# Performance work log

Measured on AMD Instinct MI355X. Metric: run time of the kernel, lower is better.

Reference implementation:

```python
import jax, jax.numpy as jnp
import numpy as np

# Soft decision tree: heap-ordered full binary tree.
# Inner node n (0-based heap index) has gate p_n = sigmoid(beta_n * (x @ W_n + b_n)).
# Children of n are 2n+1 (left, prob 1-p) and 2n+2 (right, prob p).

LMBDA = 0.1


def setup_inputs() -> dict:
    key = jax.random.key(0)
    k = jax.random.split(key, 6)
    B, IN, OUT, D = 8192, 2048, 100, 8
    N = 2 ** D - 1          # inner nodes = 255
    L = 2 ** D              # leaves = 256
    x = jax.random.normal(k[0], (B, IN), dtype=jnp.float32)
    labels = jax.random.randint(k[1], (B,), 0, OUT, dtype=jnp.int32)
    W = jax.random.normal(k[2], (N, IN), dtype=jnp.float32) * 0.02
    b = jax.random.normal(k[3], (N,), dtype=jnp.float32) * 0.02
    beta = jax.random.normal(k[4], (N,), dtype=jnp.float32)
    leaf_params = jax.random.normal(k[5], (L, OUT), dtype=jnp.float32)
    return {"x": x, "labels": labels, "W": W, "b": b, "beta": beta,
            "leaf_params": leaf_params}


def _tree_paths(p, depth):
    """p: [B, N] gate probs in heap order. Returns (inner_path [B,N], leaf_path [B,L])."""
    B = p.shape[0]
    path = jnp.ones((B, 1), p.dtype)
    inner_paths = []
    start = 0
    for d in range(depth):
        width = 2 ** d
        p_lvl = p[:, start:start + width]          # [B, width]
        inner_paths.append(path)                   # path prob arriving at each inner node
        left = path * (1.0 - p_lvl)
        right = path * p_lvl
        # interleave -> heap order of next level: [l0, r0, l1, r1, ...]
        path = jnp.stack([left, right], axis=-1).reshape(B, 2 * width)
        start += width
    return jnp.concatenate(inner_paths, axis=1), path


def reference(x, labels, W, b, beta, leaf_params):
    N = W.shape[0]
    D = int(np.log2(N + 1))            # max_depth
    OUT = leaf_params.shape[1]

    # All inner-node gates in one GEMM: sigmoid(beta * (x @ W^T + b))
    p = jax.nn.sigmoid(beta[None, :] * (x @ W.T + b[None, :]))   # [B, N]
    inner_path, leaf_path = _tree_paths(p, D)                    # [B,N], [B,L]

    # Leaf distributions: softmax over each leaf's params
    logQ = jax.nn.log_softmax(leaf_params, axis=-1)              # [L, OUT]
    Q = jnp.exp(logQ)                                            # [L, OUT]

    # y one-hot; TQ[b, l] = y_b . log Q_l
    y = jax.nn.one_hot(labels, OUT, dtype=x.dtype)               # [B, OUT]
    TQ = y @ logQ.T                                              # [B, L]
    loss = jnp.mean(jnp.sum(leaf_path * TQ, axis=1))
    neg_loss = -loss

    # Penalty: only inner nodes whose children are also inner (depth 1..D-1)
    n_pen = 2 ** (D - 1) - 1
    alpha = jnp.sum(p * inner_path, axis=0) / jnp.sum(inner_path, axis=0)  # [N]
    node_idx = np.arange(N)
    depths = np.floor(np.log2(node_idx + 1)).astype(np.int32) + 1
    lmbda_arr = jnp.asarray(LMBDA * (2.0 ** (-depths)), dtype=x.dtype)     # [N]
    a = alpha[:n_pen]
    C = -jnp.sum(lmbda_arr[:n_pen] * 0.5 * (jnp.log(a) + jnp.log1p(-a)))

    # Output: leaf distribution of the max-path-prob leaf per sample
    best_leaf = jnp.argmax(leaf_path, axis=1)                    # [B]
    output = Q[best_leaf]                                        # [B, OUT]

    return neg_loss, output, C
```

## Files before the change

kernel.cpp:

```cpp
#include <hip/hip_runtime.h>
#include <math.h>

typedef __attribute__((ext_vector_type(4)))  short short4v;
typedef __attribute__((ext_vector_type(8)))  short short8v;
typedef __attribute__((ext_vector_type(4)))  float f32x4;

#define OFF_LOGQT 256
#define OFF_Q     25856
#define OFF_WHI   51456
#define OFF_WLO   313600
#define OFF_P0    575744
#define PART_STRIDE 2097152

__device__ __forceinline__ unsigned short f2bf(float f) {
    unsigned int b = __float_as_uint(f);
    unsigned int r = (b + 0x7FFFu + ((b >> 16) & 1u)) >> 16;
    return (unsigned short)r;
}
__device__ __forceinline__ float bf2f(unsigned short u) {
    return __uint_as_float(((unsigned int)u) << 16);
}

__global__ __launch_bounds__(256) void k_prep(const float* __restrict__ W,
                                              unsigned short* __restrict__ whi,
                                              unsigned short* __restrict__ wlo,
                                              const float* __restrict__ lp,
                                              float* __restrict__ logQT,
                                              float* __restrict__ Q,
                                              float* __restrict__ accum)
{
    const int bx = blockIdx.x, tid = threadIdx.x;
    if (bx < 256) {
        if (bx == 0) accum[tid] = 0.f;
        int g = (bx * 256 + tid) * 8;
        int row = g >> 11;
        unsigned short h[8], l[8];
        if (row < 255) {
            const float* src = W + (size_t)row * 2048 + (g & 2047);
            float4 v0 = *(const float4*)src;
            float4 v1 = *(const float4*)(src + 4);
            float vv[8] = {v0.x, v0.y, v0.z, v0.w, v1.x, v1.y, v1.z, v1.w};
#pragma unroll
            for (int j = 0; j < 8; ++j) {
                h[j] = f2bf(vv[j]);
                l[j] = f2bf(vv[j] - bf2f(h[j]));
            }
        } else {
#pragma unroll
            for (int j = 0; j < 8; ++j) { h[j] = 0; l[j] = 0; }
        }
#pragma unroll
        for (int j = 0; j < 8; ++j) { whi[g + j] = h[j]; wlo[g + j] = l[j]; }
    } else {
        int w = tid >> 6, lane = tid & 63;
        int r = (bx - 256) * 4 + w;
        float v0 = (lane < 100)      ? lp[r * 100 + lane]      : -INFINITY;
        float v1 = (lane + 64 < 100) ? lp[r * 100 + lane + 64] : -INFINITY;
        float m = fmaxf(v0, v1);
        for (int s = 32; s; s >>= 1) m = fmaxf(m, __shfl_xor(m, s));
        float e = 0.f;
        if (lane < 100)      e += expf(v0 - m);
        if (lane + 64 < 100) e += expf(v1 - m);
        for (int s = 32; s; s >>= 1) e += __shfl_xor(e, s);
        float logZ = m + logf(e);
        if (lane < 100) {
            float lq = v0 - logZ;
            Q[r * 100 + lane] = expf(lq);
            logQT[lane * 256 + r] = lq;
        }
        if (lane + 64 < 100) {
            float lq = v1 - logZ;
            Q[r * 100 + lane + 64] = expf(lq);
            logQT[(lane + 64) * 256 + r] = lq;
        }
    }
}

#define GBK 64
#define LDR 136

__global__ __launch_bounds__(256, 1) void k_gemm(const float* __restrict__ x,
                                                 const unsigned short* __restrict__ whi,
                                                 const unsigned short* __restrict__ wlo,
                                                 float* __restrict__ part,
                                                 int ksteps)
{
    __shared__ unsigned short As[128 * LDR];
    __shared__ unsigned short Bs[128 * LDR];

    const int tid  = threadIdx.x;
    const int w    = tid >> 6, lane = tid & 63;
    const int wm   = w >> 1, wn = w & 1;
    const int r16  = lane & 15, hi8 = (lane >> 4) * 8;
    const int row0 = blockIdx.x * 128;
    const int col0 = blockIdx.y * 128;
    const int kz   = blockIdx.z;
    const size_t kbase = (size_t)kz * ksteps * GBK;
    float* pdst = part + (size_t)kz * PART_STRIDE;

    f32x4 acc[4][4] = {};

    float4  aR[8];
    short8v bH[4], bL[4];

    auto GL = [&](int s) {
        const size_t k0 = kbase + (size_t)s * GBK;
#pragma unroll
        for (int i = 0; i < 8; ++i) {
            int g = tid + i * 256;
            int ar = g >> 4, ac = (g & 15) * 4;
            aR[i] = *(const float4*)(x + (size_t)(row0 + ar) * 2048 + k0 + ac);
        }
#pragma unroll
        for (int i = 0; i < 4; ++i) {
            int g = tid + i * 256;
            int br = g >> 3, bc = (g & 7) * 8;
            size_t wo = (size_t)(col0 + br) * 2048 + k0 + bc;
            bH[i] = *(const short8v*)(whi + wo);
            bL[i] = *(const short8v*)(wlo + wo);
        }
    };

    auto DSW = [&]() {
#pragma unroll
        for (int i = 0; i < 8; ++i) {
            int g = tid + i * 256;
            int ar = g >> 4, ac = (g & 15) * 4;
            float vv[4] = {aR[i].x, aR[i].y, aR[i].z, aR[i].w};
            short4v hv, lv;
#pragma unroll
            for (int j = 0; j < 4; ++j) {
                unsigned short hb = f2bf(vv[j]);
                hv[j] = (short)hb;
                lv[j] = (short)f2bf(vv[j] - bf2f(hb));
            }
            *(short4v*)&As[ar * LDR + ac]      = hv;
            *(short4v*)&As[ar * LDR + 64 + ac] = lv;
        }
#pragma unroll
        for (int i = 0; i < 4; ++i) {
            int g = tid + i * 256;
            int br = g >> 3, bc = (g & 7) * 8;
            *(short8v*)&Bs[br * LDR + bc]      = bH[i];
            *(short8v*)&Bs[br * LDR + 64 + bc] = bL[i];
        }
    };

    GL(0);
    for (int s = 0; s < ksteps; ++s) {
        DSW();
        __syncthreads();
        if (s + 1 < ksteps) GL(s + 1);
#pragma unroll
        for (int kk = 0; kk < 2; ++kk) {
            const int kc = kk * 32 + hi8;
            short8v ah[4], al[4];
#pragma unroll
            for (int fm = 0; fm < 4; ++fm) {
                int base = (wm * 64 + fm * 16 + r16) * LDR + kc;
                ah[fm] = *(const short8v*)&As[base];
                al[fm] = *(const short8v*)&As[base + 64];
            }
#pragma unroll
            for (int fn = 0; fn < 4; ++fn) {
                int bb = (wn * 64 + fn * 16 + r16) * LDR + kc;
                short8v bhh = *(const short8v*)&Bs[bb];
                short8v bll = *(const short8v*)&Bs[bb + 64];
#pragma unroll
                for (int fm = 0; fm < 4; ++fm) {
                    acc[fm][fn] = __builtin_amdgcn_mfma_f32_16x16x32_bf16(ah[fm], bhh, acc[fm][fn], 0, 0, 0);
                    acc[fm][fn] = __builtin_amdgcn_mfma_f32_16x16x32_bf16(ah[fm], bll, acc[fm][fn], 0, 0, 0);
                    acc[fm][fn] = __builtin_amdgcn_mfma_f32_16x16x32_bf16(al[fm], bhh, acc[fm][fn], 0, 0, 0);
                }
            }
        }
        __syncthreads();
    }

#pragma unroll
    for (int fm = 0; fm < 4; ++fm) {
#pragma unroll
        for (int fn = 0; fn < 4; ++fn) {
            int col = col0 + wn * 64 + fn * 16 + r16;
#pragma unroll
            for (int j = 0; j < 4; ++j) {
                int row = row0 + wm * 64 + fm * 16 + (lane >> 4) * 4 + j;
                pdst[(size_t)row * 256 + col] = acc[fm][fn][j];
            }
        }
    }
}

__global__ __launch_bounds__(256) void k_tree(const float* __restrict__ part, int npart,
                                              const float* __restrict__ bias,
                                              const float* __restrict__ beta,
                                              const int* __restrict__ labels,
                                              const float* __restrict__ logQT,
                                              const float* __restrict__ Q,
                                              float* __restrict__ accum,
                                              float* __restrict__ out)
{
    __shared__ float psh[4][256];
    __shared__ float redPI[4][128];
    __shared__ float redI[4][128];
    __shared__ float lossw[4];
    const int tid = threadIdx.x;
    const int w = tid >> 6, lane = tid & 63;
    const int c0 = lane * 4;

    float4 bi, be;
    if (lane < 63) {
        bi = *(const float4*)&bias[c0];
        be = *(const float4*)&beta[c0];
    } else {
        bi = make_float4(bias[252], bias[253], bias[254], 0.f);
        be = make_float4(beta[252], beta[253], beta[254], 0.f);
    }

    float aPI0 = 0.f, aPI1 = 0.f, aI0 = 0.f, aI1 = 0.f, lossAcc = 0.f;

    for (int rr = 0; rr < 2; ++rr) {
        int b = blockIdx.x * 8 + w * 2 + rr;

        float4 s = make_float4(0.f, 0.f, 0.f, 0.f);
        for (int z = 0; z < npart; ++z) {
            float4 v = *(const float4*)&part[(size_t)z * PART_STRIDE + (size_t)b * 256 + c0];
            s.x += v.x; s.y += v.y; s.z += v.z; s.w += v.w;
        }
        float4 pv;
        pv.x = 1.f / (1.f + expf(-be.x * (s.x + bi.x)));
        pv.y = 1.f / (1.f + expf(-be.y * (s.y + bi.y)));
        pv.z = 1.f / (1.f + expf(-be.z * (s.z + bi.z)));
        pv.w = 1.f / (1.f + expf(-be.w * (s.w + bi.w)));
        *(float4*)&psh[w][c0] = pv;
        asm volatile("s_waitcnt lgkmcnt(0)" ::: "memory");
        __builtin_amdgcn_sched_barrier(0);

        int label = labels[b];
        float4 tq = *(const float4*)&logQT[(size_t)label * 256 + c0];

        float prefix = 1.f;
#pragma unroll
        for (int d = 0; d < 6; ++d) {
            int node = (1 << d) - 1 + (lane >> (6 - d));
            float g = psh[w][node];
            prefix *= ((lane >> (5 - d)) & 1) ? g : (1.f - g);
        }
        float g6  = psh[w][63 + lane];
        float p60 = prefix * (1.f - g6), p61 = prefix * g6;
        float g7a = psh[w][127 + 2 * lane];
        float g7b = psh[w][128 + 2 * lane];
        float f0 = p60 * (1.f - g7a), f1 = p60 * g7a;
        float f2 = p61 * (1.f - g7b), f3 = p61 * g7b;

        float lsum = f0 * tq.x + f1 * tq.y + f2 * tq.z + f3 * tq.w;

        float best = f0; int bestIdx = c0;
        if (f1 > best) { best = f1; bestIdx = c0 + 1; }
        if (f2 > best) { best = f2; bestIdx = c0 + 2; }
        if (f3 > best) { best = f3; bestIdx = c0 + 3; }

        for (int sft = 32; sft; sft >>= 1) lsum += __shfl_xor(lsum, sft);
        for (int sft = 32; sft; sft >>= 1) {
            float ov = __shfl_xor(best, sft);
            int   oi = __shfl_xor(bestIdx, sft);
            if (ov > best || (ov == best && oi < bestIdx)) { best = ov; bestIdx = oi; }
        }
        lossAcc += lsum;

        {
            int n = lane;
            float f = 1.f;
            int cur = n;
            while (cur > 0) {
                int par = (cur - 1) >> 1;
                float g = psh[w][par];
                f *= (cur == 2 * par + 2) ? g : (1.f - g);
                cur = par;
            }
            aPI0 += psh[w][n] * f;
            aI0  += f;
        }
        if (lane < 63) {
            int n = lane + 64;
            float f = 1.f;
            int cur = n;
            while (cur > 0) {
                int par = (cur - 1) >> 1;
                float g = psh[w][par];
                f *= (cur == 2 * par + 2) ? g : (1.f - g);
                cur = par;
            }
            aPI1 += psh[w][n] * f;
            aI1  += f;
        }

        const float* qrow = Q + (size_t)bestIdx * 100;
        float* orow = out + 1 + (size_t)b * 100;
        orow[lane] = qrow[lane];
        if (lane < 36) orow[64 + lane] = qrow[64 + lane];
    }

    redPI[w][lane] = aPI0;           redI[w][lane] = aI0;
    redPI[w][64 + lane] = (lane < 63) ? aPI1 : 0.f;
    redI [w][64 + lane] = (lane < 63) ? aI1  : 0.f;
    if (lane == 0) lossw[w] = lossAcc;
    __syncthreads();
    if (tid < 127) {
        float sPI = redPI[0][tid] + redPI[1][tid] + redPI[2][tid] + redPI[3][tid];
        float sI  = redI [0][tid] + redI [1][tid] + redI [2][tid] + redI [3][tid];
        atomicAdd(&accum[1 + tid],   sPI);
        atomicAdd(&accum[128 + tid], sI);
    }
    if (tid == 128) {
        atomicAdd(&accum[0], lossw[0] + lossw[1] + lossw[2] + lossw[3]);
    }
}

__global__ __launch_bounds__(128) void k_final(const float* __restrict__ accum,
                                               float* __restrict__ out)
{
    __shared__ float s[128];
    int t = threadIdx.x;
    float term = 0.f;
    if (t < 127) {
        float a = accum[1 + t] / accum[128 + t];
        int depth = 32 - __clz(t + 1);
        float lmbda = 0.1f * exp2f(-(float)depth);
        term = -lmbda * 0.5f * (logf(a) + log1pf(-a));
    }
    s[t] = term;
    __syncthreads();
    if (t == 0) {
        float c = 0.f;
        for (int i = 0; i < 127; ++i) c += s[i];
        out[819201] = c;
        out[0] = -accum[0] / 8192.0f;
    }
}

extern "C" void kernel_launch(void* const* d_in, const int* in_sizes, int n_in,
                              void* d_out, int out_size, void* d_ws, size_t ws_size,
                              hipStream_t stream)
{
    const float* x      = (const float*)d_in[0];
    const int*   labels = (const int*)  d_in[1];
    const float* W      = (const float*)d_in[2];
    const float* bias   = (const float*)d_in[3];
    const float* beta   = (const float*)d_in[4];
    const float* leaf   = (const float*)d_in[5];
    float* out = (float*)d_out;
    float* ws  = (float*)d_ws;

    float*          accum = ws;
    float*          logQT = ws + OFF_LOGQT;
    float*          Q     = ws + OFF_Q;
    unsigned short* whi   = (unsigned short*)(ws + OFF_WHI);
    unsigned short* wlo   = (unsigned short*)(ws + OFF_WLO);
    float*          part  = ws + OFF_P0;

    auto need = [](int k) {
        return (size_t)(OFF_P0 + (size_t)k * PART_STRIDE) * sizeof(float);
    };
    int ksplit = (ws_size >= need(4)) ? 4 : (ws_size >= need(2)) ? 2 : 1;
    int ksteps = 32 / ksplit;

    k_prep<<<320, 256, 0, stream>>>(W, whi, wlo, leaf, logQT, Q, accum);
    k_gemm<<<dim3(64, 2, ksplit), 256, 0, stream>>>(x, whi, wlo, part, ksteps);
    k_tree<<<1024, 256, 0, stream>>>(part, ksplit, bias, beta, labels, logQT, Q, accum, out);
    k_final<<<1, 128, 0, stream>>>(accum, out);
}
```

Baseline: 194.0 us.

## Pre-split x into bf16 hi/lo and stream GEMM tiles via global_load_lds

Adds a prep pass that converts x into bf16 hi/lo arrays once, so the GEMM no longer does per-tile fp32-to-bf16 splitting in registers. A new GEMM kernel uses 64x256 tiles with direct global-to-LDS loads and two blocks per CU, keeping the old kernel as a fallback when the workspace is too small. The tree kernel now processes four rows per wave in half as many blocks. The cost is an extra full read and write of x (about 64MB of traffic), and the new GEMM has no software pipelining and unpadded LDS rows, so bank conflicts are possible.

```diff
diff --git a/kernel.cpp b/kernel.cpp
--- a/kernel.cpp
+++ b/kernel.cpp
@@ -9,7 +9,10 @@
 #define OFF_Q     25856
 #define OFF_WHI   51456
 #define OFF_WLO   313600
-#define OFF_P0    575744
+#define OFF_XHI   575744
+#define OFF_XLO   8964352
+#define OFF_PART_NEW 17352960
+#define OFF_PART_OLD 575744
 #define PART_STRIDE 2097152
 
 __device__ __forceinline__ unsigned short f2bf(float f) {
@@ -20,8 +23,17 @@
 __device__ __forceinline__ float bf2f(unsigned short u) {
     return __uint_as_float(((unsigned int)u) << 16);
 }
-
-__global__ __launch_bounds__(256) void k_prep(const float* __restrict__ W,
+__device__ __forceinline__ void gl16(const void* g, void* l) {
+    __builtin_amdgcn_global_load_lds(
+        (const __attribute__((address_space(1))) unsigned int*)g,
+        (__attribute__((address_space(3))) unsigned int*)l, 16, 0, 0);
+}
+
+__global__ __launch_bounds__(256) void k_prep(const float* __restrict__ x,
+                                              unsigned short* __restrict__ xhi,
+                                              unsigned short* __restrict__ xlo,
+                                              int nxblk,
+                                              const float* __restrict__ W,
                                               unsigned short* __restrict__ whi,
                                               unsigned short* __restrict__ wlo,
                                               const float* __restrict__ lp,
@@ -30,9 +42,27 @@
                                               float* __restrict__ accum)
 {
     const int bx = blockIdx.x, tid = threadIdx.x;
-    if (bx < 256) {
-        if (bx == 0) accum[tid] = 0.f;
-        int g = (bx * 256 + tid) * 8;
+    if (bx < nxblk) {
+        int g = bx * 2048 + tid * 8;
+        float4 v0 = *(const float4*)(x + g);
+        float4 v1 = *(const float4*)(x + g + 4);
+        float vv[8] = {v0.x, v0.y, v0.z, v0.w, v1.x, v1.y, v1.z, v1.w};
+        short4v h0, h1, l0, l1;
+#pragma unroll
+        for (int j = 0; j < 4; ++j) {
+            unsigned short hb = f2bf(vv[j]);
+            h0[j] = (short)hb; l0[j] = (short)f2bf(vv[j] - bf2f(hb));
+            unsigned short hb2 = f2bf(vv[j + 4]);
+            h1[j] = (short)hb2; l1[j] = (short)f2bf(vv[j + 4] - bf2f(hb2));
+        }
+        *(short4v*)(xhi + g) = h0;  *(short4v*)(xhi + g + 4) = h1;
+        *(short4v*)(xlo + g) = l0;  *(short4v*)(xlo + g + 4) = l1;
+        return;
+    }
+    const int bxx = bx - nxblk;
+    if (bxx < 256) {
+        if (bxx == 0) accum[tid] = 0.f;
+        int g = (bxx * 256 + tid) * 8;
         int row = g >> 11;
         unsigned short h[8], l[8];
         if (row < 255) {
@@ -53,7 +83,7 @@
         for (int j = 0; j < 8; ++j) { whi[g + j] = h[j]; wlo[g + j] = l[j]; }
     } else {
         int w = tid >> 6, lane = tid & 63;
-        int r = (bx - 256) * 4 + w;
+        int r = (bxx - 256) * 4 + w;
         float v0 = (lane < 100)      ? lp[r * 100 + lane]      : -INFINITY;
         float v1 = (lane + 64 < 100) ? lp[r * 100 + lane + 64] : -INFINITY;
         float m = fmaxf(v0, v1);
@@ -76,18 +106,92 @@
     }
 }
 
+__global__ __launch_bounds__(256, 2) void k_gemm2(const unsigned short* __restrict__ xhi,
+                                                  const unsigned short* __restrict__ xlo,
+                                                  const unsigned short* __restrict__ whi,
+                                                  const unsigned short* __restrict__ wlo,
+                                                  float* __restrict__ part,
+                                                  int ksteps)
+{
+    __shared__ __align__(16) unsigned short Ah[64 * 64];
+    __shared__ __align__(16) unsigned short Al[64 * 64];
+    __shared__ __align__(16) unsigned short Bh[256 * 64];
+    __shared__ __align__(16) unsigned short Bl[256 * 64];
+
+    const int tid = threadIdx.x;
+    const int w = tid >> 6, lane = tid & 63;
+    const int r16 = lane & 15, hb = lane >> 4;
+    const int row0 = blockIdx.x * 64;
+    const int kz = blockIdx.z;
+    float* pdst = part + (size_t)kz * PART_STRIDE;
+
+    f32x4 acc[4][4] = {};
+
+    for (int s = 0; s < ksteps; ++s) {
+        const int k0 = (kz * ksteps + s) * 64;
+#pragma unroll
+        for (int it = 0; it < 2; ++it) {
+            int ch = it * 256 + tid;
+            int r = ch >> 3, c = (ch & 7) * 8;
+            gl16(xhi + (size_t)(row0 + r) * 2048 + k0 + c, &Ah[ch * 8]);
+            gl16(xlo + (size_t)(row0 + r) * 2048 + k0 + c, &Al[ch * 8]);
+        }
+#pragma unroll
+        for (int it = 0; it < 8; ++it) {
+            int ch = it * 256 + tid;
+            int r = ch >> 3, c = (ch & 7) * 8;
+            gl16(whi + (size_t)r * 2048 + k0 + c, &Bh[ch * 8]);
+            gl16(wlo + (size_t)r * 2048 + k0 + c, &Bl[ch * 8]);
+        }
+        __syncthreads();
+#pragma unroll
+        for (int kk = 0; kk < 2; ++kk) {
+            const int kc = kk * 32 + hb * 8;
+            short8v ah[4], al[4];
+#pragma unroll
+            for (int fm = 0; fm < 4; ++fm) {
+                ah[fm] = *(const short8v*)&Ah[(fm * 16 + r16) * 64 + kc];
+                al[fm] = *(const short8v*)&Al[(fm * 16 + r16) * 64 + kc];
+            }
+#pragma unroll
+            for (int fn = 0; fn < 4; ++fn) {
+                int br = w * 64 + fn * 16 + r16;
+                short8v bhh = *(const short8v*)&Bh[br * 64 + kc];
+                short8v bll = *(const short8v*)&Bl[br * 64 + kc];
+#pragma unroll
+                for (int fm = 0; fm < 4; ++fm) {
+                    acc[fm][fn] = __builtin_amdgcn_mfma_f32_16x16x32_bf16(ah[fm], bhh, acc[fm][fn], 0, 0, 0);
+                    acc[fm][fn] = __builtin_amdgcn_mfma_f32_16x16x32_bf16(ah[fm], bll, acc[fm][fn], 0, 0, 0);
+                    acc[fm][fn] = __builtin_amdgcn_mfma_f32_16x16x32_bf16(al[fm], bhh, acc[fm][fn], 0, 0, 0);
+                }
+            }
+        }
+        __syncthreads();
+    }
+
+#pragma unroll
+    for (int fm = 0; fm < 4; ++fm)
+#pragma unroll
+        for (int fn = 0; fn < 4; ++fn) {
+            int col = w * 64 + fn * 16 + r16;
+#pragma unroll
+            for (int j = 0; j < 4; ++j) {
+                int row = row0 + fm * 16 + hb * 4 + j;
+                pdst[(size_t)row * 256 + col] = acc[fm][fn][j];
+            }
+        }
+}
+
 #define GBK 64
 #define LDR 136
-
-__global__ __launch_bounds__(256, 1) void k_gemm(const float* __restrict__ x,
-                                                 const unsigned short* __restrict__ whi,
-                                                 const unsigned short* __restrict__ wlo,
-                                                 float* __restrict__ part,
-                                                 int ksteps)
+__global__ __launch_bounds__(256, 1) void k_gemm_fb(const float* __restrict__ x,
+                                                    const unsigned short* __restrict__ whi,
+                                                    const unsigned short* __restrict__ wlo,
+                                                    float* __restrict__ part,
+                                                    int ksteps)
 {
     __shared__ unsigned short As[128 * LDR];
     __shared__ unsigned short Bs[128 * LDR];
-
     const int tid  = threadIdx.x;
     const int w    = tid >> 6, lane = tid & 63;
     const int wm   = w >> 1, wn = w & 1;
@@ -97,12 +201,9 @@
     const int kz   = blockIdx.z;
     const size_t kbase = (size_t)kz * ksteps * GBK;
     float* pdst = part + (size_t)kz * PART_STRIDE;
-
     f32x4 acc[4][4] = {};
-
     float4  aR[8];
     short8v bH[4], bL[4];
-
     auto GL = [&](int s) {
         const size_t k0 = kbase + (size_t)s * GBK;
 #pragma unroll
@@ -120,7 +221,6 @@
             bL[i] = *(const short8v*)(wlo + wo);
         }
     };
-
     auto DSW = [&]() {
 #pragma unroll
         for (int i = 0; i < 8; ++i) {
@@ -130,9 +230,9 @@
             short4v hv, lv;
 #pragma unroll
             for (int j = 0; j < 4; ++j) {
-                unsigned short hb = f2bf(vv[j]);
-                hv[j] = (short)hb;
-                lv[j] = (short)f2bf(vv[j] - bf2f(hb));
+                unsigned short hbv = f2bf(vv[j]);
+                hv[j] = (short)hbv;
+                lv[j] = (short)f2bf(vv[j] - bf2f(hbv));
             }
             *(short4v*)&As[ar * LDR + ac]      = hv;
             *(short4v*)&As[ar * LDR + 64 + ac] = lv;
@@ -145,7 +245,6 @@
             *(short8v*)&Bs[br * LDR + 64 + bc] = bL[i];
         }
     };
-
     GL(0);
     for (int s = 0; s < ksteps; ++s) {
         DSW();
@@ -176,9 +275,8 @@
         }
         __syncthreads();
     }
-
-#pragma unroll
-    for (int fm = 0; fm < 4; ++fm) {
+#pragma unroll
+    for (int fm = 0; fm < 4; ++fm)
 #pragma unroll
         for (int fn = 0; fn < 4; ++fn) {
             int col = col0 + wn * 64 + fn * 16 + r16;
@@ -188,7 +286,6 @@
                 pdst[(size_t)row * 256 + col] = acc[fm][fn][j];
             }
         }
-    }
 }
 
 __global__ __launch_bounds__(256) void k_tree(const float* __restrict__ part, int npart,
@@ -219,8 +316,8 @@
 
     float aPI0 = 0.f, aPI1 = 0.f, aI0 = 0.f, aI1 = 0.f, lossAcc = 0.f;
 
-    for (int rr = 0; rr < 2; ++rr) {
-        int b = blockIdx.x * 8 + w * 2 + rr;
+    for (int rr = 0; rr < 4; ++rr) {
+        int b = blockIdx.x * 16 + w * 4 + rr;
 
         float4 s = make_float4(0.f, 0.f, 0.f, 0.f);
         for (int z = 0; z < npart; ++z) {
@@ -357,16 +454,29 @@
     float*          Q     = ws + OFF_Q;
     unsigned short* whi   = (unsigned short*)(ws + OFF_WHI);
     unsigned short* wlo   = (unsigned short*)(ws + OFF_WLO);
-    float*          part  = ws + OFF_P0;
-
-    auto need = [](int k) {
-        return (size_t)(OFF_P0 + (size_t)k * PART_STRIDE) * sizeof(float);
-    };
-    int ksplit = (ws_size >= need(4)) ? 4 : (ws_size >= need(2)) ? 2 : 1;
-    int ksteps = 32 / ksplit;
-
-    k_prep<<<320, 256, 0, stream>>>(W, whi, wlo, leaf, logQT, Q, accum);
-    k_gemm<<<dim3(64, 2, ksplit), 256, 0, stream>>>(x, whi, wlo, part, ksteps);
-    k_tree<<<1024, 256, 0, stream>>>(part, ksplit, bias, beta, labels, logQT, Q, accum, out);
+    unsigned short* xhi   = (unsigned short*)(ws + OFF_XHI);
+    unsigned short* xlo   = (unsigned short*)(ws + OFF_XLO);
+
+    auto needN = [](int k) { return (size_t)(OFF_PART_NEW + (size_t)k * PART_STRIDE) * sizeof(float); };
+    auto needO = [](int k) { return (size_t)(OFF_PART_OLD + (size_t)k * PART_STRIDE) * sizeof(float); };
+
+    int mode, ksplit;
+    if      (ws_size >= needN(4)) { mode = 2; ksplit = 4; }
+    else if (ws_size >= needN(2)) { mode = 2; ksplit = 2; }
+    else if (ws_size >= needN(1)) { mode = 2; ksplit = 1; }
+    else if (ws_size >= needO(4)) { mode = 1; ksplit = 4; }
+    else if (ws_size >= needO(2)) { mode = 1; ksplit = 2; }
+    else                          { mode = 1; ksplit = 1; }
+
+    float* part = ws + (mode == 2 ? OFF_PART_NEW : OFF_PART_OLD);
+    const int nxblk = (mode == 2) ? 8192 : 0;
+
+    k_prep<<<nxblk + 320, 256, 0, stream>>>(x, xhi, xlo, nxblk, W, whi, wlo, leaf, logQT, Q, accum);
+    if (mode == 2) {
+        k_gemm2<<<dim3(128, 1, ksplit), 256, 0, stream>>>(xhi, xlo, whi, wlo, part, 32 / ksplit);
+    } else {
+        k_gemm_fb<<<dim3(64, 2, ksplit), 256, 0, stream>>>(x, whi, wlo, part, 32 / ksplit);
+    }
+    k_tree<<<512, 256, 0, stream>>>(part, ksplit, bias, beta, labels, logQT, Q, accum, out);
     k_final<<<1, 128, 0, stream>>>(accum, out);
 }
```

Measured after the change: 178.8 us. 7.9% less time.

## Restructure split-bf16 GEMM to full-width tiles with direct-to-LDS swizzled weight loads

Applied to the files above, without the earlier changes.

The GEMM now uses 64-row by 256-column tiles, so each block covers every tree node. Each slice of x is therefore loaded and split into bf16 hi/lo only once, instead of once per column block. The weight hi/lo buffers are written by the prep kernel in an XOR-swizzled layout and streamed straight into LDS with global_load_lds, which avoids register staging and LDS bank conflicts. The explicit register prefetch of the next k-step is dropped; the design relies instead on two resident blocks per CU, which fills most of the available LDS. The tree kernel also handles 4 rows per wave with half as many blocks.

```diff
diff --git a/kernel.cpp b/kernel.cpp
--- a/kernel.cpp
+++ b/kernel.cpp
@@ -9,7 +9,7 @@
 #define OFF_Q     25856
 #define OFF_WHI   51456
 #define OFF_WLO   313600
-#define OFF_P0    575744
+#define OFF_PART  575744
 #define PART_STRIDE 2097152
 
 __device__ __forceinline__ unsigned short f2bf(float f) {
@@ -19,6 +19,11 @@
 }
 __device__ __forceinline__ float bf2f(unsigned short u) {
     return __uint_as_float(((unsigned int)u) << 16);
+}
+__device__ __forceinline__ void gl16(const void* g, void* l) {
+    __builtin_amdgcn_global_load_lds(
+        (const __attribute__((address_space(1))) unsigned int*)g,
+        (__attribute__((address_space(3))) unsigned int*)l, 16, 0, 0);
 }
 
 __global__ __launch_bounds__(256) void k_prep(const float* __restrict__ W,
@@ -34,9 +39,11 @@
         if (bx == 0) accum[tid] = 0.f;
         int g = (bx * 256 + tid) * 8;
         int row = g >> 11;
+        int c   = g & 2047;
+        int sc  = c ^ ((row & 7) << 3);
         unsigned short h[8], l[8];
         if (row < 255) {
-            const float* src = W + (size_t)row * 2048 + (g & 2047);
+            const float* src = W + (size_t)row * 2048 + c;
             float4 v0 = *(const float4*)src;
             float4 v1 = *(const float4*)(src + 4);
             float vv[8] = {v0.x, v0.y, v0.z, v0.w, v1.x, v1.y, v1.z, v1.w};
@@ -49,8 +56,9 @@
 #pragma unroll
             for (int j = 0; j < 8; ++j) { h[j] = 0; l[j] = 0; }
         }
-#pragma unroll
-        for (int j = 0; j < 8; ++j) { whi[g + j] = h[j]; wlo[g + j] = l[j]; }
+        size_t dst = (size_t)row * 2048 + sc;
+#pragma unroll
+        for (int j = 0; j < 8; ++j) { whi[dst + j] = h[j]; wlo[dst + j] = l[j]; }
     } else {
         int w = tid >> 6, lane = tid & 63;
         int r = (bx - 256) * 4 + w;
@@ -76,96 +84,76 @@
     }
 }
 
-#define GBK 64
-#define LDR 136
-
-__global__ __launch_bounds__(256, 1) void k_gemm(const float* __restrict__ x,
-                                                 const unsigned short* __restrict__ whi,
-                                                 const unsigned short* __restrict__ wlo,
-                                                 float* __restrict__ part,
-                                                 int ksteps)
-{
-    __shared__ unsigned short As[128 * LDR];
-    __shared__ unsigned short Bs[128 * LDR];
-
-    const int tid  = threadIdx.x;
-    const int w    = tid >> 6, lane = tid & 63;
-    const int wm   = w >> 1, wn = w & 1;
-    const int r16  = lane & 15, hi8 = (lane >> 4) * 8;
-    const int row0 = blockIdx.x * 128;
-    const int col0 = blockIdx.y * 128;
-    const int kz   = blockIdx.z;
-    const size_t kbase = (size_t)kz * ksteps * GBK;
+__global__ __launch_bounds__(256, 2) void k_gemm3(const float* __restrict__ x,
+                                                  const unsigned short* __restrict__ whi,
+                                                  const unsigned short* __restrict__ wlo,
+                                                  float* __restrict__ part,
+                                                  int ksteps)
+{
+    __shared__ __align__(16) unsigned short Ah[64 * 64];
+    __shared__ __align__(16) unsigned short Al[64 * 64];
+    __shared__ __align__(16) unsigned short Bh[256 * 64];
+    __shared__ __align__(16) unsigned short Bl[256 * 64];
+
+    const int tid = threadIdx.x;
+    const int w = tid >> 6, lane = tid & 63;
+    const int r16 = lane & 15, hb = lane >> 4;
+    const int row0 = blockIdx.x * 64;
+    const int kz = blockIdx.z;
     float* pdst = part + (size_t)kz * PART_STRIDE;
 
     f32x4 acc[4][4] = {};
-
-    float4  aR[8];
-    short8v bH[4], bL[4];
-
-    auto GL = [&](int s) {
-        const size_t k0 = kbase + (size_t)s * GBK;
-#pragma unroll
-        for (int i = 0; i < 8; ++i) {
-            int g = tid + i * 256;
-            int ar = g >> 4, ac = (g & 15) * 4;
-            aR[i] = *(const float4*)(x + (size_t)(row0 + ar) * 2048 + k0 + ac);
-        }
-#pragma unroll
-        for (int i = 0; i < 4; ++i) {
-            int g = tid + i * 256;
-            int br = g >> 3, bc = (g & 7) * 8;
-            size_t wo = (size_t)(col0 + br) * 2048 + k0 + bc;
-            bH[i] = *(const short8v*)(whi + wo);
-            bL[i] = *(const short8v*)(wlo + wo);
-        }
-    };
-
-    auto DSW = [&]() {
-#pragma unroll
-        for (int i = 0; i < 8; ++i) {
-            int g = tid + i * 256;
-            int ar = g >> 4, ac = (g & 15) * 4;
-            float vv[4] = {aR[i].x, aR[i].y, aR[i].z, aR[i].w};
+    float4 aR[4];
+
+    for (int s = 0; s < ksteps; ++s) {
+        const int k0 = (kz * ksteps + s) * 64;
+#pragma unroll
+        for (int it = 0; it < 4; ++it) {
+            int ch = it * 256 + tid;
+            int r = ch >> 4, c = (ch & 15) * 4;
+            aR[it] = *(const float4*)(x + (size_t)(row0 + r) * 2048 + k0 + c);
+        }
+#pragma unroll
+        for (int it = 0; it < 8; ++it) {
+            int ch = it * 256 + tid;
+            int r = ch >> 3, c = (ch & 7) * 8;
+            gl16(whi + (size_t)r * 2048 + k0 + c, &Bh[ch * 8]);
+            gl16(wlo + (size_t)r * 2048 + k0 + c, &Bl[ch * 8]);
+        }
+#pragma unroll
+        for (int it = 0; it < 4; ++it) {
+            int ch = it * 256 + tid;
+            int r = ch >> 4, c = (ch & 15) * 4;
+            int sc = c ^ ((r & 7) << 3);
+            float vv[4] = {aR[it].x, aR[it].y, aR[it].z, aR[it].w};
             short4v hv, lv;
 #pragma unroll
             for (int j = 0; j < 4; ++j) {
-                unsigned short hb = f2bf(vv[j]);
-                hv[j] = (short)hb;
-                lv[j] = (short)f2bf(vv[j] - bf2f(hb));
-            }
-            *(short4v*)&As[ar * LDR + ac]      = hv;
-            *(short4v*)&As[ar * LDR + 64 + ac] = lv;
-        }
-#pragma unroll
-        for (int i = 0; i < 4; ++i) {
-            int g = tid + i * 256;
-            int br = g >> 3, bc = (g & 7) * 8;
-            *(short8v*)&Bs[br * LDR + bc]      = bH[i];
-            *(short8v*)&Bs[br * LDR + 64 + bc] = bL[i];
-        }
-    };
-
-    GL(0);
-    for (int s = 0; s < ksteps; ++s) {
-        DSW();
+                unsigned short hbv = f2bf(vv[j]);
+                hv[j] = (short)hbv;
+                lv[j] = (short)f2bf(vv[j] - bf2f(hbv));
+            }
+            *(short4v*)&Ah[r * 64 + sc] = hv;
+            *(short4v*)&Al[r * 64 + sc] = lv;
+        }
         __syncthreads();
-        if (s + 1 < ksteps) GL(s + 1);
 #pragma unroll
         for (int kk = 0; kk < 2; ++kk) {
-            const int kc = kk * 32 + hi8;
+            const int kc = kk * 32 + hb * 8;
             short8v ah[4], al[4];
 #pragma unroll
             for (int fm = 0; fm < 4; ++fm) {
-                int base = (wm * 64 + fm * 16 + r16) * LDR + kc;
-                ah[fm] = *(const short8v*)&As[base];
-                al[fm] = *(const short8v*)&As[base + 64];
+                int r = fm * 16 + r16;
+                int idx = r * 64 + (kc ^ ((r & 7) << 3));
+                ah[fm] = *(const short8v*)&Ah[idx];
+                al[fm] = *(const short8v*)&Al[idx];
             }
 #pragma unroll
             for (int fn = 0; fn < 4; ++fn) {
-                int bb = (wn * 64 + fn * 16 + r16) * LDR + kc;
-                short8v bhh = *(const short8v*)&Bs[bb];
-                short8v bll = *(const short8v*)&Bs[bb + 64];
+                int br = w * 64 + fn * 16 + r16;
+                int bidx = br * 64 + (kc ^ ((br & 7) << 3));
+                short8v bhh = *(const short8v*)&Bh[bidx];
+                short8v bll = *(const short8v*)&Bl[bidx];
 #pragma unroll
                 for (int fm = 0; fm < 4; ++fm) {
                     acc[fm][fn] = __builtin_amdgcn_mfma_f32_16x16x32_bf16(ah[fm], bhh, acc[fm][fn], 0, 0, 0);
@@ -178,17 +166,16 @@
     }
 
 #pragma unroll
-    for (int fm = 0; fm < 4; ++fm) {
+    for (int fm = 0; fm < 4; ++fm)
 #pragma unroll
         for (int fn = 0; fn < 4; ++fn) {
-            int col = col0 + wn * 64 + fn * 16 + r16;
+            int col = w * 64 + fn * 16 + r16;
 #pragma unroll
             for (int j = 0; j < 4; ++j) {
-                int row = row0 + wm * 64 + fm * 16 + (lane >> 4) * 4 + j;
+                int row = row0 + fm * 16 + hb * 4 + j;
                 pdst[(size_t)row * 256 + col] = acc[fm][fn][j];
             }
         }
-    }
 }
 
 __global__ __launch_bounds__(256) void k_tree(const float* __restrict__ part, int npart,
@@ -219,8 +206,8 @@
 
     float aPI0 = 0.f, aPI1 = 0.f, aI0 = 0.f, aI1 = 0.f, lossAcc = 0.f;
 
-    for (int rr = 0; rr < 2; ++rr) {
-        int b = blockIdx.x * 8 + w * 2 + rr;
+    for (int rr = 0; rr < 4; ++rr) {
+        int b = blockIdx.x * 16 + w * 4 + rr;
 
         float4 s = make_float4(0.f, 0.f, 0.f, 0.f);
         for (int z = 0; z < npart; ++z) {
@@ -357,16 +344,13 @@
     float*          Q     = ws + OFF_Q;
     unsigned short* whi   = (unsigned short*)(ws + OFF_WHI);
     unsigned short* wlo   = (unsigned short*)(ws + OFF_WLO);
-    float*          part  = ws + OFF_P0;
-
-    auto need = [](int k) {
-        return (size_t)(OFF_P0 + (size_t)k * PART_STRIDE) * sizeof(float);
-    };
+    float*          part  = ws + OFF_PART;
+
+    auto need = [](int k) { return (size_t)(OFF_PART + (size_t)k * PART_STRIDE) * sizeof(float); };
     int ksplit = (ws_size >= need(4)) ? 4 : (ws_size >= need(2)) ? 2 : 1;
-    int ksteps = 32 / ksplit;
 
     k_prep<<<320, 256, 0, stream>>>(W, whi, wlo, leaf, logQT, Q, accum);
-    k_gemm<<<dim3(64, 2, ksplit), 256, 0, stream>>>(x, whi, wlo, part, ksteps);
-    k_tree<<<1024, 256, 0, stream>>>(part, ksplit, bias, beta, labels, logQT, Q, accum, out);
+    k_gemm3<<<dim3(128, 1, ksplit), 256, 0, stream>>>(x, whi, wlo, part, 32 / ksplit);
+    k_tree<<<512, 256, 0, stream>>>(part, ksplit, bias, beta, labels, logQT, Q, accum, out);
     k_final<<<1, 128, 0, stream>>>(accum, out);
 }
```

Result: faster. 163.2 us (-15.9%).
